# Performance work log

Measured on AMD Instinct MI355X. Metric: run time of the kernel, lower is better.

The kernel has to match this reference:

```python
import jax, jax.numpy as jnp
import numpy as np

SIG = [1, 1, 1, 1, -1]  # Cl(4,1)
NVEC = 5
GA = 1 << NVEC  # 32


def _build_gp_table():
    # Cayley table for the geometric product on blades indexed by bitmask.
    G = np.zeros((GA, GA, GA), np.float32)
    for a in range(GA):
        for b in range(GA):
            s = 0
            t = a >> 1
            while t:
                s += bin(t & b).count('1')
                t >>= 1
            sign = -1.0 if (s & 1) else 1.0
            common = a & b
            for i in range(NVEC):
                if (common >> i) & 1:
                    sign *= SIG[i]
            G[a, b, a ^ b] = sign
    return G

GP_TABLE = jnp.asarray(_build_gp_table())


def geometric_product(x, y):
    return jnp.einsum('...i,...j,ijk->...k', x, y, GP_TABLE)


def manifold_norm(x):
    # normalize each multivector onto the unit sphere in R^32
    return x / (jnp.linalg.norm(x, axis=-1, keepdims=True) + 1e-6)


def versor_linear(x, W, b):
    # channel mixing shared across multivector components: x [..., in, ga]
    return jnp.einsum('...ig,oi->...og', x, W) + b


def layer_norm2d(x, w, b):
    # LayerNorm over last two dims [D, ga] jointly
    mu = jnp.mean(x, axis=(-2, -1), keepdims=True)
    var = jnp.var(x, axis=(-2, -1), keepdims=True)
    return (x - mu) / jnp.sqrt(var + 1e-5) * w + b


def attention(x, Wq, bq, Wk, bk, Wv, bv, Wo, bo, n_heads):
    B, S, D, G = x.shape
    dh = D // n_heads
    q = versor_linear(x, Wq, bq).reshape(B, S, n_heads, dh, G)
    k = versor_linear(x, Wk, bk).reshape(B, S, n_heads, dh, G)
    v = versor_linear(x, Wv, bv).reshape(B, S, n_heads, dh, G)
    scale = 1.0 / np.sqrt(dh * G).astype(np.float32)
    scores = jnp.einsum('bshdg,bthdg->bhst', q, k) * scale
    probs = jax.nn.softmax(scores, axis=-1)
    o = jnp.einsum('bhst,bthdg->bshdg', probs, v).reshape(B, S, D, G)
    return versor_linear(o, Wo, bo)


N_HEADS = 8


def forward(x, Wq, bq, Wk, bk, Wv, bv, Wo, bo, ln1_w, ln1_b, ln2_w, ln2_b,
            gamma1, gamma2, W1, b1, W2, b2, Wr, br, Wc, bc):
    L = Wq.shape[0]
    for l in range(L):
        h = attention(layer_norm2d(x, ln1_w[l], ln1_b[l]),
                      Wq[l], bq[l], Wk[l], bk[l], Wv[l], bv[l], Wo[l], bo[l], N_HEADS)
        x = manifold_norm(x + gamma1[l] * h)
        m = versor_linear(layer_norm2d(x, ln2_w[l], ln2_b[l]), W1[l], b1[l])
        m = versor_linear(jnp.tanh(m), W2[l], b2[l])
        x = manifold_norm(x + gamma2[l] * m)
    # RecursiveRotorAccumulator: log(S)-step inclusive scan of rotors
    delta = versor_linear(x, Wr, br)
    rot = 0.5 * delta
    rot = rot.at[..., 0].add(1.0)
    rot = manifold_norm(rot)
    S = x.shape[1]
    step = 1
    while step < S:
        left = rot[:, :-step]
        right = rot[:, step:]
        comb = manifold_norm(geometric_product(right, left))
        rot = jnp.concatenate([rot[:, :step], comb], axis=1)
        step *= 2
    pooled = rot[:, -1]  # [B, D, ga]
    logits = pooled.reshape(pooled.shape[0], -1) @ Wc.T + bc
    return logits


def setup_inputs() -> dict:
    key = jax.random.key(0)
    B, S, D, G, L, NC = 8, 256, 64, GA, 4, 1000
    E = 4 * D  # expansion hidden
    ks = jax.random.split(key, 16)
    sd = 0.02
    inp = {
        'x': jax.random.normal(ks[0], (B, S, D, G), jnp.float32),
        'Wq': jax.random.normal(ks[1], (L, D, D), jnp.float32) * sd,
        'bq': jnp.zeros((L, D, G), jnp.float32),
        'Wk': jax.random.normal(ks[2], (L, D, D), jnp.float32) * sd,
        'bk': jnp.zeros((L, D, G), jnp.float32),
        'Wv': jax.random.normal(ks[3], (L, D, D), jnp.float32) * sd,
        'bv': jnp.zeros((L, D, G), jnp.float32),
        'Wo': jax.random.normal(ks[4], (L, D, D), jnp.float32) * sd,
        'bo': jnp.zeros((L, D, G), jnp.float32),
        'ln1_w': jnp.ones((L, D, G), jnp.float32),
        'ln1_b': jnp.zeros((L, D, G), jnp.float32),
        'ln2_w': jnp.ones((L, D, G), jnp.float32),
        'ln2_b': jnp.zeros((L, D, G), jnp.float32),
        'gamma1': 1e-5 * jnp.ones((L, D, G), jnp.float32),
        'gamma2': 1e-5 * jnp.ones((L, D, G), jnp.float32),
        'W1': jax.random.normal(ks[5], (L, E, D), jnp.float32) * sd,
        'b1': jnp.zeros((L, E, G), jnp.float32),
        'W2': jax.random.normal(ks[6], (L, D, E), jnp.float32) * sd,
        'b2': jnp.zeros((L, D, G), jnp.float32),
        'Wr': jax.random.normal(ks[7], (D, D), jnp.float32) * sd,
        'br': jnp.zeros((D, G), jnp.float32),
        'Wc': jax.random.normal(ks[8], (NC, D * G), jnp.float32) * sd,
        'bc': jnp.zeros((NC,), jnp.float32),
    }
    return inp


def reference(x, Wq, bq, Wk, bk, Wv, bv, Wo, bo, ln1_w, ln1_b, ln2_w, ln2_b,
              gamma1, gamma2, W1, b1, W2, b2, Wr, br, Wc, bc):
    return forward(x, Wq, bq, Wk, bk, Wv, bv, Wo, bo, ln1_w, ln1_b, ln2_w, ln2_b,
                   gamma1, gamma2, W1, b1, W2, b2, Wr, br, Wc, bc)
```

## Files before the change

kernel.cpp:

```cpp
#include <hip/hip_runtime.h>
#include <hip/hip_bf16.h>

constexpr int kB  = 8;
constexpr int kS  = 256;
constexpr int kD  = 64;
constexpr int kG  = 32;
constexpr int kE  = 256;
constexpr int kNH = 8;
constexpr int kHD = 256;
constexpr int kDG = kD * kG;
constexpr int kT  = kB * kS;
constexpr int kNC = 1000;

using bf16x8 = __attribute__((ext_vector_type(8))) short;
using f32x4  = __attribute__((ext_vector_type(4))) float;

__device__ __forceinline__ short f2bf(float f) {
    unsigned u = __float_as_uint(f);
    unsigned r = (u + 0x7FFFu + ((u >> 16) & 1u)) >> 16;
    return (short)r;
}

__device__ __forceinline__ float tanh_fast(float x) {
    float a = fabsf(x);
    float e = __expf(-2.f * a);
    float d = 1.f + e;
    float r = __builtin_amdgcn_rcpf(d);
    r = r * (2.f - d * r);
    float t = (1.f - e) * r;
    return copysignf(t, x);
}

__global__ __launch_bounds__(256) void cvtw_kernel(
    const float* __restrict__ Wq, const float* __restrict__ Wk,
    const float* __restrict__ Wv, const float* __restrict__ Wo,
    const float* __restrict__ W1, const float* __restrict__ W2,
    unsigned short* __restrict__ dst) {
    int idx = (blockIdx.x * 256 + threadIdx.x) * 4;
    const float* src; int off;
    if      (idx <  16384) { src = Wq; off = 0; }
    else if (idx <  32768) { src = Wk; off = 16384; }
    else if (idx <  49152) { src = Wv; off = 32768; }
    else if (idx <  65536) { src = Wo; off = 49152; }
    else if (idx < 131072) { src = W1; off = 65536; }
    else                   { src = W2; off = 131072; }
    const float4 v = *(const float4*)(src + (idx - off));
    *(short4*)&dst[idx] = make_short4(f2bf(v.x), f2bf(v.y), f2bf(v.z), f2bf(v.w));
}

__global__ __launch_bounds__(256) void prep_tr_kernel(
    const float* __restrict__ bq, const float* __restrict__ bk,
    const float* __restrict__ bv, const float* __restrict__ bo,
    const float* __restrict__ b2, const float* __restrict__ gm1,
    const float* __restrict__ gm2, const float* __restrict__ ln2w,
    const float* __restrict__ ln2b, const float* __restrict__ ln1w,
    const float* __restrict__ ln1b, const float* __restrict__ b1,
    float* __restrict__ dst) {
    __shared__ float lt[32 * 257];
    const int a = blockIdx.x >> 2, l = blockIdx.x & 3;
    const float* srcs[12] = {bq, bk, bv, bo, b2, gm1, gm2, ln2w, ln2b, ln1w, ln1b, b1};
    const int R  = (a == 11) ? 256 : 64;
    const int sh = (a == 11) ? 8 : 6;
    const float* src = srcs[a] + (size_t)l * R * 32;
    float* out = dst + a * 8192 + l * R * 32;
    const int tid = threadIdx.x;
    for (int j = tid; j < R * 32; j += 256) lt[(j & 31) * (R + 1) + (j >> 5)] = src[j];
    __syncthreads();
    for (int k = tid; k < R * 32; k += 256) {
        int g = k >> sh, r = k & (R - 1);
        out[k] = lt[g * (R + 1) + r];
    }
}

__global__ __launch_bounds__(256) void ln_kernel(const float* __restrict__ Xin,
                                                 const float* __restrict__ w,
                                                 const float* __restrict__ b,
                                                 unsigned short* __restrict__ A,
                                                 float* __restrict__ XT) {
    int t = blockIdx.x, tid = threadIdx.x;
    const float* xp = Xin + (size_t)t * kDG;
    __shared__ float r1[256], r2[256];
    __shared__ short st[32 * 72];
    __shared__ float xf[32 * 68];
    float v[8], s = 0.f, ss = 0.f;
#pragma unroll
    for (int j = 0; j < 8; j++) {
        float x = xp[tid + j * 256];
        v[j] = x; s += x; ss += x * x;
        int jj = tid + j * 256;
        xf[(jj & 31) * 68 + (jj >> 5)] = x;
    }
    r1[tid] = s; r2[tid] = ss; __syncthreads();
    for (int o = 128; o > 0; o >>= 1) {
        if (tid < o) { r1[tid] += r1[tid + o]; r2[tid] += r2[tid + o]; }
        __syncthreads();
    }
    float mean = r1[0] * (1.f / kDG);
    float var  = r2[0] * (1.f / kDG) - mean * mean;
    float rstd = rsqrtf(var + 1e-5f);
#pragma unroll
    for (int j = 0; j < 8; j++) {
        int jj = tid + j * 256;
        float val = (v[j] - mean) * rstd * w[jj] + b[jj];
        st[(jj & 31) * 72 + (jj >> 5)] = f2bf(val);
    }
    __syncthreads();
    bf16x8 ov = *(const bf16x8*)&st[(tid >> 3) * 72 + (tid & 7) * 8];
    *(bf16x8*)&A[(size_t)t * kDG + tid * 8] = ov;
    const int row = tid >> 3, col = (tid & 7) * 8;
    float* xo = XT + (size_t)t * kDG + tid * 8;
    *(float4*)(xo + 0) = *(const float4*)&xf[row * 68 + col + 0];
    *(float4*)(xo + 4) = *(const float4*)&xf[row * 68 + col + 4];
}

__global__ __launch_bounds__(256) void vlinT_kernel(const float* __restrict__ XT,
                                                    const float* __restrict__ W,
                                                    const float* __restrict__ bias,
                                                    float* __restrict__ OutT) {
    __shared__ float sx[32 * 65];
    __shared__ float sw[kD * kD];
    int t = blockIdx.x, tid = threadIdx.x;
    const float* xp = XT + (size_t)t * kDG;
    for (int j = tid; j < kDG; j += 256) sx[(j >> 6) * 65 + (j & 63)] = xp[j];
    for (int j = tid; j < kD * kD; j += 256) sw[j] = W[j];
    __syncthreads();
    int g = tid & 31, ob = tid >> 5;
    int b = t >> 8, s = t & 255;
    float* op = OutT + ((size_t)b * kD * kS + s) * kG;
    for (int o = ob; o < kD; o += 8) {
        float acc = bias[o * kG + g];
        const float* wr = sw + o * kD;
#pragma unroll
        for (int i = 0; i < kD; i++) acc += wr[i] * sx[g * 65 + i];
        op[(size_t)o * kS * kG + g] = acc;
    }
}

template<bool LAST>
__global__ __launch_bounds__(256, 2) void mega_kernel(
    const unsigned short* __restrict__ O,
    const unsigned short* __restrict__ Woh, const float* __restrict__ boT,
    const float* __restrict__ gm1T,
    const float* __restrict__ ln2wT, const float* __restrict__ ln2bT,
    const unsigned short* __restrict__ W1h, const float* __restrict__ b1T,
    const unsigned short* __restrict__ W2h, const float* __restrict__ b2T,
    const float* __restrict__ gm2T,
    const float* __restrict__ ln1wT, const float* __restrict__ ln1bT,
    float* __restrict__ XT,
    const unsigned short* __restrict__ Wqh, const unsigned short* __restrict__ Wkh,
    const unsigned short* __restrict__ Wvh,
    const float* __restrict__ bqT, const float* __restrict__ bkT,
    const float* __restrict__ bvT,
    unsigned short* __restrict__ Q, unsigned short* __restrict__ K,
    unsigned short* __restrict__ V) {
    constexpr int AS = 72;
    constexpr int MS = 264;
    __shared__ short sA[32 * AS];
    __shared__ short sM[32 * MS];
    __shared__ float sred[8];

    const int tid = threadIdx.x;
    const int w = tid >> 6, lane = tid & 63;
    const int l16 = lane & 15, quad = lane >> 4;
    const int tok = blockIdx.x;
    const size_t tb = (size_t)tok * kDG;
    const int o0 = w * 16 + quad * 4;

    float xv[2][4];
    bf16x8 w1f[8];
    {
        const unsigned short* xp = O + tb;
        bf16x8 bfr[2][2];
#pragma unroll
        for (int c = 0; c < 2; ++c)
#pragma unroll
            for (int nt = 0; nt < 2; ++nt)
                bfr[c][nt] = *(const bf16x8*)&xp[(nt * 16 + l16) * kD + c * 32 + quad * 8];

        f32x4 accW[2];
#pragma unroll
        for (int nt = 0; nt < 2; ++nt) accW[nt] = (f32x4){0.f, 0.f, 0.f, 0.f};
#pragma unroll
        for (int c = 0; c < 2; ++c) {
            bf16x8 afr = *(const bf16x8*)&Woh[(w * 16 + l16) * kD + c * 32 + quad * 8];
#pragma unroll
            for (int nt = 0; nt < 2; ++nt)
                accW[nt] = __builtin_amdgcn_mfma_f32_16x16x32_bf16(afr, bfr[c][nt], accW[nt], 0, 0, 0);
        }

#pragma unroll
        for (int mt = 0; mt < 4; ++mt)
#pragma unroll
            for (int c = 0; c < 2; ++c)
                w1f[mt * 2 + c] = *(const bf16x8*)&W1h[((w * 4 + mt) * 16 + l16) * kD + c * 32 + quad * 8];

        float s = 0.f, ss = 0.f;
        float vv[2][4];
#pragma unroll
        for (int nt = 0; nt < 2; ++nt) {
            int g = nt * 16 + l16;
            const float4 b4 = *(const float4*)&boT[g * kD + o0];
            const float4 g4 = *(const float4*)&gm1T[g * kD + o0];
            const float4 xi = *(const float4*)&XT[tb + g * kD + o0];
#pragma unroll
            for (int r = 0; r < 4; ++r)
                vv[nt][r] = (&xi.x)[r] + (&g4.x)[r] * (accW[nt][r] + (&b4.x)[r]);
        }
#pragma unroll
        for (int r = 0; r < 4; ++r) {
            float sq = vv[0][r] * vv[0][r] + vv[1][r] * vv[1][r];
#pragma unroll
            for (int off = 1; off < 16; off <<= 1) sq += __shfl_xor(sq, off, 64);
            float rn = 1.f / (sqrtf(sq) + 1e-6f);
#pragma unroll
            for (int nt = 0; nt < 2; ++nt) {
                float x = vv[nt][r] * rn;
                xv[nt][r] = x;
                s += x; ss = fmaf(x, x, ss);
            }
        }
#pragma unroll
        for (int off = 1; off < 64; off <<= 1) {
            s += __shfl_xor(s, off, 64); ss += __shfl_xor(ss, off, 64);
        }
        if (lane == 0) { sred[w] = s; sred[4 + w] = ss; }
        __syncthreads();
        float st = sred[0] + sred[1] + sred[2] + sred[3];
        float sst = sred[4] + sred[5] + sred[6] + sred[7];
        float mean = st * (1.f / kDG);
        float var  = sst * (1.f / kDG) - mean * mean;
        float rstd = rsqrtf(var + 1e-5f);
#pragma unroll
        for (int nt = 0; nt < 2; ++nt) {
            int g = nt * 16 + l16;
            const float4 w4 = *(const float4*)&ln2wT[g * kD + o0];
            const float4 b4 = *(const float4*)&ln2bT[g * kD + o0];
            short4 s4;
#pragma unroll
            for (int r = 0; r < 4; ++r)
                (&s4.x)[r] = f2bf((xv[nt][r] - mean) * rstd * (&w4.x)[r] + (&b4.x)[r]);
            *(short4*)&sA[g * AS + o0] = s4;
        }
    }
    __syncthreads();

    bf16x8 w2f[8];
    {
        bf16x8 afrA[2][2];
#pragma unroll
        for (int c = 0; c < 2; ++c)
#pragma unroll
            for (int nt = 0; nt < 2; ++nt)
                afrA[c][nt] = *(const bf16x8*)&sA[(nt * 16 + l16) * AS + c * 32 + quad * 8];

        f32x4 acc1[4][2];
#pragma unroll
        for (int mt = 0; mt < 4; ++mt)
#pragma unroll
            for (int nt = 0; nt < 2; ++nt) acc1[mt][nt] = (f32x4){0.f, 0.f, 0.f, 0.f};
#pragma unroll
        for (int mt = 0; mt < 4; ++mt)
#pragma unroll
            for (int c = 0; c < 2; ++c)
#pragma unroll
                for (int nt = 0; nt < 2; ++nt)
                    acc1[mt][nt] = __builtin_amdgcn_mfma_f32_16x16x32_bf16(w1f[mt * 2 + c], afrA[c][nt], acc1[mt][nt], 0, 0, 0);

#pragma unroll
        for (int c = 0; c < 8; ++c)
            w2f[c] = *(const bf16x8*)&W2h[(w * 16 + l16) * kE + c * 32 + quad * 8];

#pragma unroll
        for (int mt = 0; mt < 4; ++mt)
#pragma unroll
            for (int nt = 0; nt < 2; ++nt) {
                int g = nt * 16 + l16;
                int e0 = (w * 4 + mt) * 16 + quad * 4;
                const float4 b4 = *(const float4*)&b1T[g * kE + e0];
                short4 s4;
#pragma unroll
                for (int r = 0; r < 4; ++r)
                    (&s4.x)[r] = f2bf(tanh_fast(acc1[mt][nt][r] + (&b4.x)[r]));
                *(short4*)&sM[g * MS + e0] = s4;
            }
    }
    __syncthreads();

    f32x4 acc2[2];
#pragma unroll
    for (int nt = 0; nt < 2; ++nt) acc2[nt] = (f32x4){0.f, 0.f, 0.f, 0.f};
#pragma unroll
    for (int c = 0; c < 8; ++c) {
        bf16x8 bq[2];
#pragma unroll
        for (int nt = 0; nt < 2; ++nt)
            bq[nt] = *(const bf16x8*)&sM[(nt * 16 + l16) * MS + c * 32 + quad * 8];
#pragma unroll
        for (int nt = 0; nt < 2; ++nt)
            acc2[nt] = __builtin_amdgcn_mfma_f32_16x16x32_bf16(w2f[c], bq[nt], acc2[nt], 0, 0, 0);
    }

    bf16x8 wqf[6];
    if constexpr (!LAST) {
        const unsigned short* Wp[3] = {Wqh, Wkh, Wvh};
#pragma unroll
        for (int m = 0; m < 3; ++m)
#pragma unroll
            for (int c = 0; c < 2; ++c)
                wqf[m * 2 + c] = *(const bf16x8*)&Wp[m][(w * 16 + l16) * kD + c * 32 + quad * 8];
    }

    float yv[2][4];
    float s2 = 0.f, ss2 = 0.f;
    {
        float vv[2][4];
#pragma unroll
        for (int nt = 0; nt < 2; ++nt) {
            int g = nt * 16 + l16;
            const float4 b4 = *(const float4*)&b2T[g * kD + o0];
            const float4 g4 = *(const float4*)&gm2T[g * kD + o0];
#pragma unroll
            for (int r = 0; r < 4; ++r)
                vv[nt][r] = xv[nt][r] + (&g4.x)[r] * (acc2[nt][r] + (&b4.x)[r]);
        }
#pragma unroll
        for (int r = 0; r < 4; ++r) {
            float sq = vv[0][r] * vv[0][r] + vv[1][r] * vv[1][r];
#pragma unroll
            for (int off = 1; off < 16; off <<= 1) sq += __shfl_xor(sq, off, 64);
            float rn = 1.f / (sqrtf(sq) + 1e-6f);
#pragma unroll
            for (int nt = 0; nt < 2; ++nt) {
                float x = vv[nt][r] * rn;
                yv[nt][r] = x;
                s2 += x; ss2 = fmaf(x, x, ss2);
            }
        }
#pragma unroll
        for (int nt = 0; nt < 2; ++nt) {
            int g = nt * 16 + l16;
            float4 xo;
#pragma unroll
            for (int r = 0; r < 4; ++r) (&xo.x)[r] = yv[nt][r];
            *(float4*)&XT[tb + g * kD + o0] = xo;
        }
    }
    if constexpr (LAST) return;

#pragma unroll
    for (int off = 1; off < 64; off <<= 1) {
        s2 += __shfl_xor(s2, off, 64); ss2 += __shfl_xor(ss2, off, 64);
    }
    if (lane == 0) { sred[w] = s2; sred[4 + w] = ss2; }
    __syncthreads();
    {
        float st = sred[0] + sred[1] + sred[2] + sred[3];
        float sst = sred[4] + sred[5] + sred[6] + sred[7];
        float mean = st * (1.f / kDG);
        float var  = sst * (1.f / kDG) - mean * mean;
        float rstd = rsqrtf(var + 1e-5f);
#pragma unroll
        for (int nt = 0; nt < 2; ++nt) {
            int g = nt * 16 + l16;
            const float4 w4 = *(const float4*)&ln1wT[g * kD + o0];
            const float4 b4 = *(const float4*)&ln1bT[g * kD + o0];
            short4 s4;
#pragma unroll
            for (int r = 0; r < 4; ++r)
                (&s4.x)[r] = f2bf((yv[nt][r] - mean) * rstd * (&w4.x)[r] + (&b4.x)[r]);
            *(short4*)&sA[g * AS + o0] = s4;
        }
    }
    __syncthreads();

    {
        bf16x8 afrA[2][2];
#pragma unroll
        for (int c = 0; c < 2; ++c)
#pragma unroll
            for (int nt = 0; nt < 2; ++nt)
                afrA[c][nt] = *(const bf16x8*)&sA[(nt * 16 + l16) * AS + c * 32 + quad * 8];

        const float* Bp[3] = {bqT, bkT, bvT};
        unsigned short* Op[3] = {Q, K, V};
#pragma unroll
        for (int m = 0; m < 3; ++m) {
            f32x4 acc3[2];
#pragma unroll
            for (int nt = 0; nt < 2; ++nt) acc3[nt] = (f32x4){0.f, 0.f, 0.f, 0.f};
#pragma unroll
            for (int c = 0; c < 2; ++c)
#pragma unroll
                for (int nt = 0; nt < 2; ++nt)
                    acc3[nt] = __builtin_amdgcn_mfma_f32_16x16x32_bf16(wqf[m * 2 + c], afrA[c][nt], acc3[nt], 0, 0, 0);
            unsigned short* op = Op[m] + tb;
#pragma unroll
            for (int nt = 0; nt < 2; ++nt) {
                int g = nt * 16 + l16;
                const float4 b4 = *(const float4*)&Bp[m][g * kD + o0];
#pragma unroll
                for (int r = 0; r < 4; ++r)
                    op[(o0 + r) * kG + g] = (unsigned short)f2bf(acc3[nt][r] + (&b4.x)[r]);
            }
        }
    }
}

__global__ __launch_bounds__(256, 3) void gemm_qkv_kernel(
    const unsigned short* __restrict__ X,
    const unsigned short* __restrict__ Wqh, const unsigned short* __restrict__ Wkh,
    const unsigned short* __restrict__ Wvh,
    const float* __restrict__ bqT, const float* __restrict__ bkT, const float* __restrict__ bvT,
    unsigned short* __restrict__ Q, unsigned short* __restrict__ K, unsigned short* __restrict__ V) {
    constexpr int WS = 64 + 8;
    __shared__ short sW[3 * 64 * WS];

    const int tid = threadIdx.x, wave = tid >> 6, lane = tid & 63;
    const int l16 = lane & 15, quad = lane >> 4;
    const int tok = blockIdx.x * 4 + wave;

    const unsigned short* Wp[3] = {Wqh, Wkh, Wvh};
#pragma unroll
    for (int w = 0; w < 3; ++w)
        for (int j = tid * 8; j < 64 * 64; j += 2048) {
            int o = j >> 6, i = j & 63;
            *(bf16x8*)&sW[w * 64 * WS + o * WS + i] = *(const bf16x8*)(Wp[w] + j);
        }

    const unsigned short* xp = X + (size_t)tok * kDG;
    bf16x8 bfr[2][2];
#pragma unroll
    for (int c = 0; c < 2; ++c)
#pragma unroll
        for (int nt = 0; nt < 2; ++nt)
            bfr[c][nt] = *(const bf16x8*)&xp[(nt * 16 + l16) * kD + c * 32 + quad * 8];
    __syncthreads();

    f32x4 acc[3][4][2];
#pragma unroll
    for (int w = 0; w < 3; ++w)
#pragma unroll
        for (int mt = 0; mt < 4; ++mt)
#pragma unroll
            for (int nt = 0; nt < 2; ++nt) acc[w][mt][nt] = (f32x4){0.f, 0.f, 0.f, 0.f};

#pragma unroll
    for (int w = 0; w < 3; ++w)
#pragma unroll
        for (int mt = 0; mt < 4; ++mt)
#pragma unroll
            for (int c = 0; c < 2; ++c) {
                bf16x8 afr = *(const bf16x8*)&sW[w * 64 * WS + (mt * 16 + l16) * WS + c * 32 + quad * 8];
#pragma unroll
                for (int nt = 0; nt < 2; ++nt)
                    acc[w][mt][nt] = __builtin_amdgcn_mfma_f32_16x16x32_bf16(afr, bfr[c][nt], acc[w][mt][nt], 0, 0, 0);
            }

    unsigned short* Op[3] = {Q, K, V};
    const float* Bp[3] = {bqT, bkT, bvT};
#pragma unroll
    for (int w = 0; w < 3; ++w) {
        unsigned short* op = Op[w] + (size_t)tok * kDG;
#pragma unroll
        for (int mt = 0; mt < 4; ++mt)
#pragma unroll
            for (int nt = 0; nt < 2; ++nt) {
                int g = nt * 16 + l16;
                int o0 = mt * 16 + quad * 4;
                const float4 b4 = *(const float4*)&Bp[w][g * kD + o0];
#pragma unroll
                for (int r = 0; r < 4; ++r)
                    op[(o0 + r) * kG + g] = (unsigned short)f2bf(acc[w][mt][nt][r] + (&b4.x)[r]);
            }
    }
}

constexpr int QSTR = 264;
constexpr int VSTR = 40;

__global__ __launch_bounds__(128) void attn_mfma_kernel(const unsigned short* __restrict__ Q,
                                                        const unsigned short* __restrict__ K,
                                                        const unsigned short* __restrict__ V,
                                                        unsigned short* __restrict__ O) {
    __shared__ short sQ[32 * QSTR];
    __shared__ short sKV[2][256 * VSTR];

    const int qt = blockIdx.x, h = blockIdx.y, b = blockIdx.z;
    const int tid = threadIdx.x;
    const int wave = tid >> 6, lane = tid & 63;
    const int l16 = lane & 15, quad = lane >> 4;

    const size_t bh = (size_t)b * kS * kDG + (size_t)h * kHD;

#pragma unroll
    for (int it = 0; it < 8; ++it) {
        int j = it * 1024 + tid * 8;
        int row = j >> 8, col = j & 255;
        *(bf16x8*)&sQ[row * QSTR + col] =
            *(const bf16x8*)(Q + bh + (size_t)(qt * 32 + row) * kDG + col);
    }
#pragma unroll
    for (int it = 0; it < 8; ++it) {
        int j = it * 1024 + tid * 8;
        int row = j >> 8, col = j & 255;
        *(bf16x8*)&sKV[0][row * QSTR + col] =
            *(const bf16x8*)(K + bh + (size_t)row * kDG + col);
    }
    __syncthreads();

    bf16x8 afrag[8];
    {
        int row = wave * 16 + l16;
#pragma unroll
        for (int c = 0; c < 8; ++c)
            afrag[c] = *(const bf16x8*)&sQ[row * QSTR + c * 32 + quad * 8];
    }

    f32x4 acc[16];
#pragma unroll
    for (int i = 0; i < 16; ++i) acc[i] = (f32x4){0.f, 0.f, 0.f, 0.f};

    for (int kt = 0; kt < 8; ++kt) {
        bf16x8 kpre[8];
        if (kt < 7) {
#pragma unroll
            for (int it = 0; it < 8; ++it) {
                int j = it * 1024 + tid * 8;
                int row = j >> 8, col = j & 255;
                kpre[it] = *(const bf16x8*)(K + bh + (size_t)((kt + 1) * 32 + row) * kDG + col);
            }
        }
        const short* kb = sKV[kt & 1];
#pragma unroll
        for (int nt = 0; nt < 2; ++nt) {
            int key = nt * 16 + l16;
            f32x4 a = acc[kt * 2 + nt];
#pragma unroll
            for (int c = 0; c < 8; ++c) {
                bf16x8 bfrag = *(const bf16x8*)&kb[key * QSTR + c * 32 + quad * 8];
                a = __builtin_amdgcn_mfma_f32_16x16x32_bf16(afrag[c], bfrag, a, 0, 0, 0);
            }
            acc[kt * 2 + nt] = a;
        }
        if (kt < 7) {
            short* nb = sKV[(kt + 1) & 1];
#pragma unroll
            for (int it = 0; it < 8; ++it) {
                int j = it * 1024 + tid * 8;
                int row = j >> 8, col = j & 255;
                *(bf16x8*)&nb[row * QSTR + col] = kpre[it];
            }
            __syncthreads();
        }
    }

    float inv[4];
#pragma unroll
    for (int r = 0; r < 4; ++r) {
        float m = -1e30f;
#pragma unroll
        for (int t = 0; t < 16; ++t) m = fmaxf(m, acc[t][r]);
#pragma unroll
        for (int off = 1; off < 16; off <<= 1) m = fmaxf(m, __shfl_xor(m, off, 16));
        float s = 0.f;
#pragma unroll
        for (int t = 0; t < 16; ++t) {
            float p = __expf((acc[t][r] - m) * 0.0625f);
            acc[t][r] = p; s += p;
        }
#pragma unroll
        for (int off = 1; off < 16; off <<= 1) s += __shfl_xor(s, off, 16);
        inv[r] = 1.f / s;
    }

#pragma unroll
    for (int t = 0; t < 16; ++t)
#pragma unroll
        for (int r = 0; r < 4; ++r)
            sQ[(wave * 16 + quad * 4 + r) * QSTR + t * 16 + l16] = f2bf(acc[t][r]);

    {
        const int db = tid & 63, kh = tid >> 6;
        short4 vr[16];
#pragma unroll
        for (int r = 0; r < 16; ++r)
            vr[r] = *(const short4*)(V + bh + (size_t)(kh * 16 + r) * kDG + db * 4);
#pragma unroll
        for (int i = 0; i < 4; ++i)
#pragma unroll
            for (int gq = 0; gq < 4; ++gq) {
                short4 p = make_short4((&vr[gq * 4 + 0].x)[i], (&vr[gq * 4 + 1].x)[i],
                                       (&vr[gq * 4 + 2].x)[i], (&vr[gq * 4 + 3].x)[i]);
                *(short4*)&sKV[0][(db * 4 + i) * VSTR + kh * 16 + gq * 4] = p;
            }
    }
    __syncthreads();

    f32x4 oacc[16];
#pragma unroll
    for (int i = 0; i < 16; ++i) oacc[i] = (f32x4){0.f, 0.f, 0.f, 0.f};

    for (int vt = 0; vt < 8; ++vt) {
        short4 vpre[16];
        if (vt < 7) {
            const int db = tid & 63, kh = tid >> 6;
#pragma unroll
            for (int r = 0; r < 16; ++r)
                vpre[r] = *(const short4*)(V + bh + (size_t)((vt + 1) * 32 + kh * 16 + r) * kDG + db * 4);
        }
        const short* vb = sKV[vt & 1];
        bf16x8 pfrag = *(const bf16x8*)&sQ[(wave * 16 + l16) * QSTR + vt * 32 + quad * 8];
#pragma unroll
        for (int dt = 0; dt < 16; ++dt) {
            bf16x8 vfrag = *(const bf16x8*)&vb[(dt * 16 + l16) * VSTR + quad * 8];
            oacc[dt] = __builtin_amdgcn_mfma_f32_16x16x32_bf16(pfrag, vfrag, oacc[dt], 0, 0, 0);
        }
        if (vt < 7) {
            const int db = tid & 63, kh = tid >> 6;
            short* nb = sKV[(vt + 1) & 1];
#pragma unroll
            for (int i = 0; i < 4; ++i)
#pragma unroll
                for (int gq = 0; gq < 4; ++gq) {
                    short4 p = make_short4((&vpre[gq * 4 + 0].x)[i], (&vpre[gq * 4 + 1].x)[i],
                                           (&vpre[gq * 4 + 2].x)[i], (&vpre[gq * 4 + 3].x)[i]);
                    *(short4*)&nb[(db * 4 + i) * VSTR + kh * 16 + gq * 4] = p;
                }
            __syncthreads();
        }
    }

    {
        const size_t ob = (size_t)(b * kS + qt * 32 + wave * 16 + quad * 4) * kDG + h * 8;
#pragma unroll
        for (int gg = 0; gg < 2; ++gg) {
            int g = gg * 16 + l16;
#pragma unroll
            for (int r = 0; r < 4; ++r) {
                bf16x8 pk;
#pragma unroll
                for (int k = 0; k < 8; ++k)
                    pk[k] = f2bf(oacc[k * 2 + gg][r] * inv[r]);
                *(bf16x8*)&O[ob + (size_t)r * kDG + g * kD] = pk;
            }
        }
    }
}

constexpr int pc_ce(unsigned v) { int c = 0; while (v) { c += v & 1; v >>= 1; } return c; }
constexpr unsigned gp_mask_ce(int a) {
    unsigned m = 0;
    for (int c = 0; c < 32; ++c) {
        int b = a ^ c;
        int s = (a & b) >> 4;
        for (int t = a >> 1; t; t >>= 1) s += pc_ce(t & b);
        if (s & 1) m |= (1u << c);
    }
    return m;
}

template<int A>
__device__ __forceinline__ void gp_term(const float* x, const float* y, float* acc) {
    constexpr unsigned m = gp_mask_ce(A);
    const float xa = x[A], nxa = -xa;
#pragma unroll
    for (int c = 0; c < 32; ++c)
        acc[c] = fmaf(((m >> c) & 1u) ? nxa : xa, y[A ^ c], acc[c]);
}

__device__ __forceinline__ void gp_mn_t(const float* x, const float* y, float* out) {
    float acc[32];
#pragma unroll
    for (int c = 0; c < 32; ++c) acc[c] = 0.f;
    gp_term<0>(x, y, acc);  gp_term<1>(x, y, acc);  gp_term<2>(x, y, acc);  gp_term<3>(x, y, acc);
    gp_term<4>(x, y, acc);  gp_term<5>(x, y, acc);  gp_term<6>(x, y, acc);  gp_term<7>(x, y, acc);
    gp_term<8>(x, y, acc);  gp_term<9>(x, y, acc);  gp_term<10>(x, y, acc); gp_term<11>(x, y, acc);
    gp_term<12>(x, y, acc); gp_term<13>(x, y, acc); gp_term<14>(x, y, acc); gp_term<15>(x, y, acc);
    gp_term<16>(x, y, acc); gp_term<17>(x, y, acc); gp_term<18>(x, y, acc); gp_term<19>(x, y, acc);
    gp_term<20>(x, y, acc); gp_term<21>(x, y, acc); gp_term<22>(x, y, acc); gp_term<23>(x, y, acc);
    gp_term<24>(x, y, acc); gp_term<25>(x, y, acc); gp_term<26>(x, y, acc); gp_term<27>(x, y, acc);
    gp_term<28>(x, y, acc); gp_term<29>(x, y, acc); gp_term<30>(x, y, acc); gp_term<31>(x, y, acc);
    float ss = 0.f;
#pragma unroll
    for (int c = 0; c < 32; ++c) ss = fmaf(acc[c], acc[c], ss);
    float r = 1.f / (sqrtf(ss) + 1e-6f);
#pragma unroll
    for (int c = 0; c < 32; ++c) out[c] = acc[c] * r;
}

__device__ __forceinline__ void leaf_load(const float* base, float* v) {
#pragma unroll
    for (int i = 0; i < 8; ++i) {
        const float4 f = *(const float4*)(base + i * 4);
        v[i * 4 + 0] = 0.5f * f.x; v[i * 4 + 1] = 0.5f * f.y;
        v[i * 4 + 2] = 0.5f * f.z; v[i * 4 + 3] = 0.5f * f.w;
    }
    v[0] += 1.f;
    float ss = 0.f;
#pragma unroll
    for (int c = 0; c < 32; ++c) ss = fmaf(v[c], v[c], ss);
    float r = 1.f / (sqrtf(ss) + 1e-6f);
#pragma unroll
    for (int c = 0; c < 32; ++c) v[c] *= r;
}

__global__ __launch_bounds__(256) void scanreg_kernel(const float* __restrict__ DT,
                                                      float* __restrict__ pooled) {
    const int wave = threadIdx.x >> 6, lane = threadIdx.x & 63;
    const int seq = blockIdx.x * 4 + wave;
    const float* base = DT + ((size_t)seq * kS + lane * 4) * kG;

    float R[32], Y[32], P[32], Xa[32], Yb[32];

    leaf_load(base, R);
    for (int j = 1; j < 4; ++j) {
        leaf_load(base + j * kG, Y);
        gp_mn_t(Y, R, R);
    }

    for (int step = 1; step < 64; step <<= 1) {
        const bool up = lane & step;
#pragma unroll
        for (int c = 0; c < 32; ++c) P[c] = __shfl_xor(R[c], step, 64);
#pragma unroll
        for (int c = 0; c < 32; ++c) {
            Xa[c] = up ? R[c] : P[c];
            Yb[c] = up ? P[c] : R[c];
        }
        gp_mn_t(Xa, Yb, R);
    }

    if (lane == 0) {
        float* op = pooled + (size_t)seq * kG;
#pragma unroll
        for (int i = 0; i < 8; ++i)
            *(float4*)(op + i * 4) = make_float4(R[i * 4], R[i * 4 + 1], R[i * 4 + 2], R[i * 4 + 3]);
    }
}

__global__ __launch_bounds__(256) void cls2_kernel(const float* __restrict__ P,
                                                   const float* __restrict__ Wc,
                                                   const float* __restrict__ bc,
                                                   float* __restrict__ out) {
    __shared__ float sp[kB * kDG];
    const int tid = threadIdx.x, wave = tid >> 6, lane = tid & 63;
    for (int j = tid * 4; j < kB * kDG; j += 1024)
        *(float4*)&sp[j] = *(const float4*)(P + j);
    __syncthreads();

    const int c = blockIdx.x * 4 + wave;
    const float* w = Wc + (size_t)c * kDG;
    float acc[kB];
#pragma unroll
    for (int b = 0; b < kB; ++b) acc[b] = 0.f;
#pragma unroll
    for (int cc = 0; cc < 8; ++cc) {
        const float4 w4 = *(const float4*)(w + cc * 256 + lane * 4);
#pragma unroll
        for (int b = 0; b < kB; ++b) {
            const float4 p4 = *(const float4*)&sp[b * kDG + cc * 256 + lane * 4];
            acc[b] += w4.x * p4.x + w4.y * p4.y + w4.z * p4.z + w4.w * p4.w;
        }
    }
#pragma unroll
    for (int b = 0; b < kB; ++b)
#pragma unroll
        for (int off = 32; off > 0; off >>= 1) acc[b] += __shfl_xor(acc[b], off, 64);
    if (lane == 0) {
        float bias = bc[c];
#pragma unroll
        for (int b = 0; b < kB; ++b) out[b * kNC + c] = acc[b] + bias;
    }
}

extern "C" void kernel_launch(void* const* d_in, const int* in_sizes, int n_in,
                              void* d_out, int out_size, void* d_ws, size_t ws_size,
                              hipStream_t stream) {
    const float* x_in = (const float*)d_in[0];
    const float* Wq   = (const float*)d_in[1];
    const float* bq   = (const float*)d_in[2];
    const float* Wk   = (const float*)d_in[3];
    const float* bk   = (const float*)d_in[4];
    const float* Wv   = (const float*)d_in[5];
    const float* bv   = (const float*)d_in[6];
    const float* Wo   = (const float*)d_in[7];
    const float* bo   = (const float*)d_in[8];
    const float* ln1w = (const float*)d_in[9];
    const float* ln1b = (const float*)d_in[10];
    const float* ln2w = (const float*)d_in[11];
    const float* ln2b = (const float*)d_in[12];
    const float* gm1  = (const float*)d_in[13];
    const float* gm2  = (const float*)d_in[14];
    const float* W1   = (const float*)d_in[15];
    const float* b1   = (const float*)d_in[16];
    const float* W2   = (const float*)d_in[17];
    const float* b2   = (const float*)d_in[18];
    const float* Wr   = (const float*)d_in[19];
    const float* br   = (const float*)d_in[20];
    const float* Wc   = (const float*)d_in[21];
    const float* bc   = (const float*)d_in[22];

    const size_t NEL = (size_t)kT * kDG;
    float* F  = (float*)d_ws;
    float* XT = F;
    unsigned short* Abf = (unsigned short*)(F + NEL);
    unsigned short* Qh = (unsigned short*)(F + 2 * NEL);
    unsigned short* Kh = (unsigned short*)(F + 3 * NEL);
    unsigned short* Vh = (unsigned short*)(F + 4 * NEL);
    unsigned short* Wb = (unsigned short*)(F + 5 * NEL);
    float* PT = F + 3 * NEL + NEL / 2;
    float* pooled = F + 2 * NEL;
    float* DT = F + NEL;

    cvtw_kernel<<<192, 256, 0, stream>>>(Wq, Wk, Wv, Wo, W1, W2, Wb);
    prep_tr_kernel<<<48, 256, 0, stream>>>(bq, bk, bv, bo, b2, gm1, gm2,
                                           ln2w, ln2b, ln1w, ln1b, b1, PT);
    unsigned short* Wqh = Wb;
    unsigned short* Wkh = Wb + 16384;
    unsigned short* Wvh = Wb + 32768;
    unsigned short* Woh = Wb + 49152;
    unsigned short* W1h = Wb + 65536;
    unsigned short* W2h = Wb + 131072;

    auto bqT   = [&](int l) { return PT + 0     + l * 2048; };
    auto bkT   = [&](int l) { return PT + 8192  + l * 2048; };
    auto bvT   = [&](int l) { return PT + 16384 + l * 2048; };
    auto boT   = [&](int l) { return PT + 24576 + l * 2048; };
    auto b2T   = [&](int l) { return PT + 32768 + l * 2048; };
    auto gm1T  = [&](int l) { return PT + 40960 + l * 2048; };
    auto gm2T  = [&](int l) { return PT + 49152 + l * 2048; };
    auto ln2wT = [&](int l) { return PT + 57344 + l * 2048; };
    auto ln2bT = [&](int l) { return PT + 65536 + l * 2048; };
    auto ln1wT = [&](int l) { return PT + 73728 + l * 2048; };
    auto ln1bT = [&](int l) { return PT + 81920 + l * 2048; };
    auto b1T   = [&](int l) { return PT + 90112 + l * 8192; };

    ln_kernel<<<kT, 256, 0, stream>>>(x_in, ln1w, ln1b, Abf, XT);
    gemm_qkv_kernel<<<kT / 4, 256, 0, stream>>>(Abf,
        Wqh, Wkh, Wvh, bqT(0), bkT(0), bvT(0), Qh, Kh, Vh);

    for (int l = 0; l < 4; l++) {
        attn_mfma_kernel<<<dim3(8, kNH, kB), 128, 0, stream>>>(Qh, Kh, Vh, Abf);
        if (l < 3)
            mega_kernel<false><<<kT, 256, 0, stream>>>(Abf,
                Woh + l * 4096, boT(l), gm1T(l), ln2wT(l), ln2bT(l),
                W1h + l * 16384, b1T(l), W2h + l * 16384, b2T(l), gm2T(l),
                ln1wT(l + 1), ln1bT(l + 1), XT,
                Wqh + (l + 1) * 4096, Wkh + (l + 1) * 4096, Wvh + (l + 1) * 4096,
                bqT(l + 1), bkT(l + 1), bvT(l + 1), Qh, Kh, Vh);
        else
            mega_kernel<true><<<kT, 256, 0, stream>>>(Abf,
                Woh + l * 4096, boT(l), gm1T(l), ln2wT(l), ln2bT(l),
                W1h + l * 16384, b1T(l), W2h + l * 16384, b2T(l), gm2T(l),
                nullptr, nullptr, XT,
                nullptr, nullptr, nullptr, nullptr, nullptr, nullptr,
                nullptr, nullptr, nullptr);
    }

    vlinT_kernel<<<kT, 256, 0, stream>>>(XT, Wr, br, DT);
    scanreg_kernel<<<kB * kD / 4, 256, 0, stream>>>(DT, pooled);
    cls2_kernel<<<kNC / 4, 256, 0, stream>>>(pooled, Wc, bc, (float*)d_out);
}
```

Baseline: 518.8 us.

## Hoist LN/bias loads, load Q fragments directly, and use one-wave scan blocks

In the mega kernel, the layer-norm weights and the QKV bias vectors are now loaded into registers early, before the reductions and barriers, so their global latency overlaps other work. In the attention kernel, Q fragments are read straight from global memory into registers instead of being staged through shared memory; the shared buffer is kept only for the probability tile. The scan kernel now launches 64-thread blocks with one sequence each instead of four waves per block, which spreads the work over more blocks. The trade-off is higher register pressure from the hoisted values.

```diff
diff --git a/kernel.cpp b/kernel.cpp
--- a/kernel.cpp
+++ b/kernel.cpp
@@ -194,6 +194,14 @@
             for (int c = 0; c < 2; ++c)
                 w1f[mt * 2 + c] = *(const bf16x8*)&W1h[((w * 4 + mt) * 16 + l16) * kD + c * 32 + quad * 8];
 
+        float4 lw2[2], lb2[2];
+#pragma unroll
+        for (int nt = 0; nt < 2; ++nt) {
+            int g = nt * 16 + l16;
+            lw2[nt] = *(const float4*)&ln2wT[g * kD + o0];
+            lb2[nt] = *(const float4*)&ln2bT[g * kD + o0];
+        }
+
         float s = 0.f, ss = 0.f;
         float vv[2][4];
 #pragma unroll
@@ -233,12 +241,10 @@
 #pragma unroll
         for (int nt = 0; nt < 2; ++nt) {
             int g = nt * 16 + l16;
-            const float4 w4 = *(const float4*)&ln2wT[g * kD + o0];
-            const float4 b4 = *(const float4*)&ln2bT[g * kD + o0];
             short4 s4;
 #pragma unroll
             for (int r = 0; r < 4; ++r)
-                (&s4.x)[r] = f2bf((xv[nt][r] - mean) * rstd * (&w4.x)[r] + (&b4.x)[r]);
+                (&s4.x)[r] = f2bf((xv[nt][r] - mean) * rstd * (&lw2[nt].x)[r] + (&lb2[nt].x)[r]);
             *(short4*)&sA[g * AS + o0] = s4;
         }
     }
@@ -301,6 +307,7 @@
     }
 
     bf16x8 wqf[6];
+    float4 lw1[2], lb1[2], pbq[2], pbk[2], pbv[2];
     if constexpr (!LAST) {
         const unsigned short* Wp[3] = {Wqh, Wkh, Wvh};
 #pragma unroll
@@ -308,6 +315,15 @@
 #pragma unroll
             for (int c = 0; c < 2; ++c)
                 wqf[m * 2 + c] = *(const bf16x8*)&Wp[m][(w * 16 + l16) * kD + c * 32 + quad * 8];
+#pragma unroll
+        for (int nt = 0; nt < 2; ++nt) {
+            int g = nt * 16 + l16;
+            lw1[nt] = *(const float4*)&ln1wT[g * kD + o0];
+            lb1[nt] = *(const float4*)&ln1bT[g * kD + o0];
+            pbq[nt] = *(const float4*)&bqT[g * kD + o0];
+            pbk[nt] = *(const float4*)&bkT[g * kD + o0];
+            pbv[nt] = *(const float4*)&bvT[g * kD + o0];
+        }
     }
 
     float yv[2][4];
@@ -362,12 +378,10 @@
 #pragma unroll
         for (int nt = 0; nt < 2; ++nt) {
             int g = nt * 16 + l16;
-            const float4 w4 = *(const float4*)&ln1wT[g * kD + o0];
-            const float4 b4 = *(const float4*)&ln1bT[g * kD + o0];
             short4 s4;
 #pragma unroll
             for (int r = 0; r < 4; ++r)
-                (&s4.x)[r] = f2bf((yv[nt][r] - mean) * rstd * (&w4.x)[r] + (&b4.x)[r]);
+                (&s4.x)[r] = f2bf((yv[nt][r] - mean) * rstd * (&lw1[nt].x)[r] + (&lb1[nt].x)[r]);
             *(short4*)&sA[g * AS + o0] = s4;
         }
     }
@@ -381,7 +395,7 @@
             for (int nt = 0; nt < 2; ++nt)
                 afrA[c][nt] = *(const bf16x8*)&sA[(nt * 16 + l16) * AS + c * 32 + quad * 8];
 
-        const float* Bp[3] = {bqT, bkT, bvT};
+        const float4* Bp[3][2] = {{&pbq[0], &pbq[1]}, {&pbk[0], &pbk[1]}, {&pbv[0], &pbv[1]}};
         unsigned short* Op[3] = {Q, K, V};
 #pragma unroll
         for (int m = 0; m < 3; ++m) {
@@ -397,7 +411,7 @@
 #pragma unroll
             for (int nt = 0; nt < 2; ++nt) {
                 int g = nt * 16 + l16;
-                const float4 b4 = *(const float4*)&Bp[m][g * kD + o0];
+                const float4 b4 = *Bp[m][nt];
 #pragma unroll
                 for (int r = 0; r < 4; ++r)
                     op[(o0 + r) * kG + g] = (unsigned short)f2bf(acc3[nt][r] + (&b4.x)[r]);
@@ -482,7 +496,7 @@
                                                         const unsigned short* __restrict__ K,
                                                         const unsigned short* __restrict__ V,
                                                         unsigned short* __restrict__ O) {
-    __shared__ short sQ[32 * QSTR];
+    __shared__ short sP[32 * QSTR];
     __shared__ short sKV[2][256 * VSTR];
 
     const int qt = blockIdx.x, h = blockIdx.y, b = blockIdx.z;
@@ -492,13 +506,14 @@
 
     const size_t bh = (size_t)b * kS * kDG + (size_t)h * kHD;
 
-#pragma unroll
-    for (int it = 0; it < 8; ++it) {
-        int j = it * 1024 + tid * 8;
-        int row = j >> 8, col = j & 255;
-        *(bf16x8*)&sQ[row * QSTR + col] =
-            *(const bf16x8*)(Q + bh + (size_t)(qt * 32 + row) * kDG + col);
-    }
+    bf16x8 afrag[8];
+    {
+        const unsigned short* qp = Q + bh + (size_t)(qt * 32 + wave * 16 + l16) * kDG;
+#pragma unroll
+        for (int c = 0; c < 8; ++c)
+            afrag[c] = *(const bf16x8*)(qp + c * 32 + quad * 8);
+    }
+
 #pragma unroll
     for (int it = 0; it < 8; ++it) {
         int j = it * 1024 + tid * 8;
@@ -508,14 +523,6 @@
     }
     __syncthreads();
 
-    bf16x8 afrag[8];
-    {
-        int row = wave * 16 + l16;
-#pragma unroll
-        for (int c = 0; c < 8; ++c)
-            afrag[c] = *(const bf16x8*)&sQ[row * QSTR + c * 32 + quad * 8];
-    }
-
     f32x4 acc[16];
 #pragma unroll
     for (int i = 0; i < 16; ++i) acc[i] = (f32x4){0.f, 0.f, 0.f, 0.f};
@@ -577,7 +584,7 @@
     for (int t = 0; t < 16; ++t)
 #pragma unroll
         for (int r = 0; r < 4; ++r)
-            sQ[(wave * 16 + quad * 4 + r) * QSTR + t * 16 + l16] = f2bf(acc[t][r]);
+            sP[(wave * 16 + quad * 4 + r) * QSTR + t * 16 + l16] = f2bf(acc[t][r]);
 
     {
         const int db = tid & 63, kh = tid >> 6;
@@ -609,7 +616,7 @@
                 vpre[r] = *(const short4*)(V + bh + (size_t)((vt + 1) * 32 + kh * 16 + r) * kDG + db * 4);
         }
         const short* vb = sKV[vt & 1];
-        bf16x8 pfrag = *(const bf16x8*)&sQ[(wave * 16 + l16) * QSTR + vt * 32 + quad * 8];
+        bf16x8 pfrag = *(const bf16x8*)&sP[(wave * 16 + l16) * QSTR + vt * 32 + quad * 8];
 #pragma unroll
         for (int dt = 0; dt < 16; ++dt) {
             bf16x8 vfrag = *(const bf16x8*)&vb[(dt * 16 + l16) * VSTR + quad * 8];
@@ -704,10 +711,10 @@
     for (int c = 0; c < 32; ++c) v[c] *= r;
 }
 
-__global__ __launch_bounds__(256) void scanreg_kernel(const float* __restrict__ DT,
-                                                      float* __restrict__ pooled) {
-    const int wave = threadIdx.x >> 6, lane = threadIdx.x & 63;
-    const int seq = blockIdx.x * 4 + wave;
+__global__ __launch_bounds__(64) void scanreg_kernel(const float* __restrict__ DT,
+                                                     float* __restrict__ pooled) {
+    const int lane = threadIdx.x & 63;
+    const int seq = blockIdx.x;
     const float* base = DT + ((size_t)seq * kS + lane * 4) * kG;
 
     float R[32], Y[32], P[32], Xa[32], Yb[32];
@@ -858,6 +865,6 @@
     }
 
     vlinT_kernel<<<kT, 256, 0, stream>>>(XT, Wr, br, DT);
-    scanreg_kernel<<<kB * kD / 4, 256, 0, stream>>>(DT, pooled);
+    scanreg_kernel<<<kB * kD, 64, 0, stream>>>(DT, pooled);
     cls2_kernel<<<kNC / 4, 256, 0, stream>>>(pooled, Wc, bc, (float*)d_out);
 }
```

Measured after the change: 510.2 us. About the same (-1.6%).
